# Kernel tuning notes

Measured on AMD Instinct MI355X. Metric: run time of the kernel, lower is better.

## Reference

```python
import jax, jax.numpy as jnp
import numpy as np

D_MODEL, N_LEVELS, N_HEADS, N_POINTS = 256, 4, 8, 4
SHAPES = [(100, 100), (50, 50), (25, 25), (13, 13)]  # (H, W) per level


def setup_inputs() -> dict:
    key = jax.random.key(0)
    ks = jax.random.split(key, 8)
    N = 2
    C = D_MODEL
    Len_in = sum(h * w for h, w in SHAPES)
    Lq = Len_in  # encoder self-attention
    query = jax.random.normal(ks[0], (N, Lq, C), jnp.float32)
    reference_points = jax.random.uniform(ks[1], (N, Lq, N_LEVELS, 2), dtype=jnp.float32)
    input_flatten = jax.random.normal(ks[2], (N, Len_in, C), jnp.float32)
    input_spatial_shapes = np.array(SHAPES, dtype=np.int64)
    areas = input_spatial_shapes[:, 0] * input_spatial_shapes[:, 1]
    input_level_start_index = np.concatenate([[0], np.cumsum(areas)[:-1]]).astype(np.int64)
    s = 1.0 / np.sqrt(C)
    Wv = jax.random.uniform(ks[3], (C, C), jnp.float32, -s, s)
    bv = jnp.zeros((C,), jnp.float32)
    # sampling_offsets: small random weight + the module's grid bias init
    Woff = jax.random.normal(ks[4], (N_HEADS * N_LEVELS * N_POINTS * 2, C), jnp.float32) * 0.01
    thetas = jnp.arange(N_HEADS, dtype=jnp.float32) * (2.0 * np.pi / N_HEADS)
    grid = jnp.stack([jnp.cos(thetas), jnp.sin(thetas)], -1)  # (M,2)
    grid = grid / jnp.max(jnp.abs(grid), axis=-1, keepdims=True)
    grid = jnp.tile(grid[:, None, None, :], (1, N_LEVELS, N_POINTS, 1))
    grid = grid * (jnp.arange(N_POINTS, dtype=jnp.float32) + 1.0)[None, None, :, None]
    boff = grid.reshape(-1)
    Wa = jax.random.normal(ks[5], (N_HEADS * N_LEVELS * N_POINTS, C), jnp.float32) * 0.02
    ba = jnp.zeros((N_HEADS * N_LEVELS * N_POINTS,), jnp.float32)
    Wo = jax.random.uniform(ks[6], (C, C), jnp.float32, -s, s)
    bo = jnp.zeros((C,), jnp.float32)
    return {
        'query': query, 'reference_points': reference_points, 'input_flatten': input_flatten,
        'input_spatial_shapes': input_spatial_shapes, 'input_level_start_index': input_level_start_index,
        'Wv': Wv, 'bv': bv, 'Woff': Woff, 'boff': boff, 'Wa': Wa, 'ba': ba, 'Wo': Wo, 'bo': bo,
    }


def _msda_forward(query, reference_points, input_flatten, shapes, starts,
                  Wv, bv, Woff, boff, Wa, ba, Wo, bo):
    N, Lq, C = query.shape
    M, L, P = N_HEADS, N_LEVELS, N_POINTS
    D = C // M
    value = (input_flatten @ Wv.T + bv).reshape(N, -1, M, D)  # (N, Len_in, M, D)
    off = (query @ Woff.T + boff).reshape(N, Lq, M, L, P, 2)
    attn = jax.nn.softmax((query @ Wa.T + ba).reshape(N, Lq, M, L * P), axis=-1)
    attn = attn.reshape(N, Lq, M, L, P)
    # offset_normalizer = (W_l, H_l)
    norm = jnp.asarray(shapes[:, ::-1].copy(), jnp.float32)  # (L, 2)
    loc = reference_points[:, :, None, :, None, :] + off / norm[None, None, None, :, None, :]
    grids = 2.0 * loc - 1.0  # (N, Lq, M, L, P, 2), grid_sample convention
    out = jnp.zeros((N, Lq, M, D), query.dtype)
    for l in range(L):
        H, W = int(shapes[l, 0]), int(shapes[l, 1])
        s0 = int(starts[l])
        v = value[:, s0:s0 + H * W]  # (N, H*W, M, D)
        # align_corners=False unnormalization
        gx = ((grids[:, :, :, l, :, 0] + 1.0) * W - 1.0) / 2.0  # (N, Lq, M, P)
        gy = ((grids[:, :, :, l, :, 1] + 1.0) * H - 1.0) / 2.0
        x0 = jnp.floor(gx); y0 = jnp.floor(gy)
        fx = gx - x0;       fy = gy - y0
        x0i = x0.astype(jnp.int32); y0i = y0.astype(jnp.int32)

        def gather(iy, ix):
            valid = (iy >= 0) & (iy < H) & (ix >= 0) & (ix < W)
            lin = jnp.clip(iy, 0, H - 1) * W + jnp.clip(ix, 0, W - 1)  # (N, Lq, M, P)
            lin2 = lin.transpose(0, 1, 3, 2).reshape(N, Lq * P, M)
            g = jnp.take_along_axis(v, lin2[..., None], axis=1)  # (N, Lq*P, M, D)
            g = g.reshape(N, Lq, P, M, D).transpose(0, 1, 3, 2, 4)  # (N, Lq, M, P, D)
            return g * valid[..., None]  # zero padding outside

        s00 = gather(y0i, x0i)
        s01 = gather(y0i, x0i + 1)
        s10 = gather(y0i + 1, x0i)
        s11 = gather(y0i + 1, x0i + 1)
        sampled = (s00 * ((1 - fy) * (1 - fx))[..., None] + s01 * ((1 - fy) * fx)[..., None]
                   + s10 * (fy * (1 - fx))[..., None] + s11 * (fy * fx)[..., None])
        out = out + jnp.einsum('nqmp,nqmpd->nqmd', attn[:, :, :, l], sampled)
    out = out.reshape(N, Lq, C)
    return out @ Wo.T + bo


def reference(query, reference_points, input_flatten, input_spatial_shapes, input_level_start_index,
              Wv, bv, Woff, boff, Wa, ba, Wo, bo):
    shapes = np.asarray(input_spatial_shapes)
    starts = np.asarray(input_level_start_index)
    return _msda_forward(query, reference_points, input_flatten, shapes, starts,
                         Wv, bv, Woff, boff, Wa, ba, Wo, bo)
```

## Files before the change

kernel.cpp:

```cpp
#include <hip/hip_runtime.h>
#include <math.h>

#define NB   2
#define LQ   13294
#define NROWS (NB*LQ)
#define CDIM 256

typedef unsigned short u16;
typedef unsigned int   u32;
typedef short bf16x8 __attribute__((ext_vector_type(8)));
typedef float f32x4  __attribute__((ext_vector_type(4)));

struct alignas(8) U16x4 { u16 x, y, z, w; };

__device__ __forceinline__ u16 f2bf(float f) {
    u32 u = __builtin_bit_cast(u32, f);
    u += 0x7FFFu + ((u >> 16) & 1u);
    return (u16)(u >> 16);
}
__device__ __forceinline__ float bf2f(u16 h) {
    u32 u = ((u32)h) << 16;
    return __builtin_bit_cast(float, u);
}

__global__ __launch_bounds__(256)
void prep_all(const float4* __restrict__ query, const float4* __restrict__ inflat,
              const float* __restrict__ Wv, const float* __restrict__ Woff,
              const float* __restrict__ Wa, const float* __restrict__ Wo,
              const float* __restrict__ boff, const float* __restrict__ ba,
              u16* __restrict__ qb, u16* __restrict__ ib,
              u16* __restrict__ wb, float* __restrict__ biascat) {
    const int b = blockIdx.x;
    const int t = threadIdx.x;
    if (b < 6647) {
        int i = b * 256 + t;
        float4 v = query[i];
        U16x4 o{f2bf(v.x), f2bf(v.y), f2bf(v.z), f2bf(v.w)};
        *(U16x4*)&qb[(size_t)i * 4] = o;
    } else if (b < 13294) {
        int i = (b - 6647) * 256 + t;
        float4 v = inflat[i];
        U16x4 o{f2bf(v.x), f2bf(v.y), f2bf(v.z), f2bf(v.w)};
        *(U16x4*)&ib[(size_t)i * 4] = o;
    } else {
        int i = (b - 13294) * 256 + t;
        float v;
        if      (i <  65536) v = Wv[i];
        else if (i < 131072) v = Woff[i - 65536];
        else if (i < 163840) v = Wa[i - 131072];
        else                 v = Wo[i - 163840];
        wb[i] = f2bf(v);
        if (b == 13294) {
            biascat[t] = boff[t];
            if (t < 128) biascat[256 + t] = ba[t];
        }
    }
}

#define GEMM_CORE(A_, B_)                                                     \
    __shared__ u16 Bs[128 * 256];                                             \
    const int tid  = threadIdx.x;                                             \
    const int wave = tid >> 6;                                                \
    const int lane = tid & 63;                                                \
    const int ln16 = lane & 15;                                               \
    const int kq   = lane >> 4;                                               \
    const int row0 = blockIdx.y * 128;                                        \
    const int wr   = (wave >> 1) * 64;                                        \
    const int wc   = (wave & 1) * 64;                                         \
    _Pragma("unroll")                                                         \
    for (int it = 0; it < 16; ++it) {                                         \
        int g  = it * 256 + tid;                                              \
        int c  = g >> 5;                                                      \
        int ch = g & 31;                                                      \
        float4 v = *(const float4*)((B_) + (size_t)c * 256 + ch * 8);         \
        *(float4*)&Bs[c * 256 + (ch ^ (c & 7)) * 8] = v;                      \
    }                                                                         \
    bf16x8 a[4][8];                                                           \
    _Pragma("unroll")                                                         \
    for (int i = 0; i < 4; ++i) {                                             \
        int gr = min(row0 + wr + i * 16 + ln16, M - 1);                       \
        const u16* Ap = (A_) + (size_t)gr * 256 + kq * 8;                     \
        _Pragma("unroll")                                                     \
        for (int kt = 0; kt < 8; ++kt)                                        \
            a[i][kt] = *(const bf16x8*)(Ap + kt * 32);                        \
    }                                                                         \
    __syncthreads();                                                          \
    f32x4 acc[4][4] = {};                                                     \
    _Pragma("unroll")                                                         \
    for (int kt = 0; kt < 8; ++kt) {                                          \
        bf16x8 bfr[4];                                                        \
        _Pragma("unroll")                                                     \
        for (int j = 0; j < 4; ++j) {                                         \
            int c2 = wc + j * 16 + ln16;                                      \
            bfr[j] = *(const bf16x8*)&Bs[c2 * 256 + ((kt * 4 + kq) ^ (c2 & 7)) * 8]; \
        }                                                                     \
        _Pragma("unroll")                                                     \
        for (int i = 0; i < 4; ++i)                                           \
            _Pragma("unroll")                                                 \
            for (int j = 0; j < 4; ++j)                                       \
                acc[i][j] = __builtin_amdgcn_mfma_f32_16x16x32_bf16(          \
                    a[i][kt], bfr[j], acc[i][j], 0, 0, 0);                    \
    }

__global__ __launch_bounds__(256, 2)
void gemm_front(const u16* __restrict__ qb, const u16* __restrict__ ib,
                const u16* __restrict__ wb, const float* __restrict__ bv,
                const float* __restrict__ bcat, u16* __restrict__ value,
                float* __restrict__ offb, float* __restrict__ logit, int M) {
    const int bx = blockIdx.x;
    const u16* Aptr = (bx < 2) ? ib : qb;
    const u16* Bptr = (bx < 2) ? (wb + (size_t)bx * 128 * 256)
                               : (wb + 65536 + (size_t)(bx - 2) * 128 * 256);
    const float* bias = (bx < 2) ? (bv + bx * 128) : (bcat + (bx - 2) * 128);

    GEMM_CORE(Aptr, Bptr)

    #pragma unroll
    for (int j = 0; j < 4; ++j) {
        int lc = wc + j * 16 + ln16;
        float bj = bias[lc];
        #pragma unroll
        for (int i = 0; i < 4; ++i) {
            int gr0 = row0 + wr + i * 16 + kq * 4;
            #pragma unroll
            for (int r = 0; r < 4; ++r) {
                int gr = gr0 + r;
                if (gr < M) {
                    float o = acc[i][j][r] + bj;
                    if (bx < 2)
                        value[(size_t)gr * 256 + bx * 128 + lc] = f2bf(o);
                    else if (bx < 4)
                        offb[(size_t)gr * 256 + (bx - 2) * 128 + lc] = o;
                    else
                        logit[(size_t)gr * 128 + lc] = o;
                }
            }
        }
    }
}

__global__ __launch_bounds__(256, 2)
void gemm_out(const u16* __restrict__ A, const u16* __restrict__ Bw,
              const float* __restrict__ bias, float* __restrict__ C, int M) {
    const u16* Bptr = Bw + (size_t)blockIdx.x * 128 * 256;
    GEMM_CORE(A, Bptr)
    #pragma unroll
    for (int j = 0; j < 4; ++j) {
        int gc = blockIdx.x * 128 + wc + j * 16 + ln16;
        float bj = bias[gc];
        #pragma unroll
        for (int i = 0; i < 4; ++i) {
            int gr0 = row0 + wr + i * 16 + kq * 4;
            #pragma unroll
            for (int r = 0; r < 4; ++r) {
                int gr = gr0 + r;
                if (gr < M) C[(size_t)gr * 256 + gc] = acc[i][j][r] + bj;
            }
        }
    }
}

__global__ __launch_bounds__(256)
void msda_sample(const u16* __restrict__ value,
                 const float* __restrict__ refpts,
                 const float* __restrict__ off,
                 const float* __restrict__ logits,
                 u16* __restrict__ tmp) {
    __shared__ float sAw[4][8][16];
    __shared__ int   sLin[4][8][17][4];
    __shared__ float sW[4][8][17][4];

    const int t  = threadIdx.x;
    const int qb = blockIdx.x * 4;

    if (t < 32) {
        const int qi = t >> 3, m = t & 7;
        const float* lg = logits + (size_t)(qb + qi) * 128 + m * 16;
        float e[16];
        float mx = -1e30f;
        #pragma unroll
        for (int i = 0; i < 16; ++i) { e[i] = lg[i]; mx = fmaxf(mx, e[i]); }
        float s = 0.f;
        #pragma unroll
        for (int i = 0; i < 16; ++i) { e[i] = __expf(e[i] - mx); s += e[i]; }
        const float inv = 1.f / s;
        #pragma unroll
        for (int i = 0; i < 16; ++i) sAw[qi][m][i] = e[i] * inv;
    }
    __syncthreads();

    #pragma unroll
    for (int j2 = 0; j2 < 2; ++j2) {
        const int job = t + j2 * 256;
        const int qi = job >> 7;
        const int m  = (job >> 4) & 7;
        const int p  = job & 15;
        const int l  = p >> 2, pp = p & 3;
        const int q  = qb + qi;
        const int n  = (q >= LQ) ? 1 : 0;

        const int W = (l == 0) ? 100 : (l == 1) ? 50 : (l == 2) ? 25 : 13;
        const int H = W;
        const int st = (l == 0) ? 0 : (l == 1) ? 10000 : (l == 2) ? 12500 : 13125;

        const float rx = refpts[(size_t)q * 8 + l * 2 + 0];
        const float ry = refpts[(size_t)q * 8 + l * 2 + 1];
        const float ox = off[(size_t)q * 256 + m * 32 + (l * 4 + pp) * 2 + 0];
        const float oy = off[(size_t)q * 256 + m * 32 + (l * 4 + pp) * 2 + 1];

        const float locx = rx + ox / (float)W;
        const float locy = ry + oy / (float)H;
        const float grx = 2.f * locx - 1.f;
        const float gry = 2.f * locy - 1.f;
        const float gx = ((grx + 1.f) * (float)W - 1.f) * 0.5f;
        const float gy = ((gry + 1.f) * (float)H - 1.f) * 0.5f;
        const float x0f = floorf(gx), y0f = floorf(gy);
        const float fx = gx - x0f, fy = gy - y0f;
        const int x0 = (int)x0f, y0 = (int)y0f;
        const int x1 = x0 + 1, y1 = y0 + 1;

        const int cx0 = min(max(x0, 0), W - 1);
        const int cx1 = min(max(x1, 0), W - 1);
        const int cy0 = min(max(y0, 0), H - 1);
        const int cy1 = min(max(y1, 0), H - 1);
        const bool vx0 = (x0 >= 0) & (x0 < W);
        const bool vx1 = (x1 >= 0) & (x1 < W);
        const bool vy0 = (y0 >= 0) & (y0 < H);
        const bool vy1 = (y1 >= 0) & (y1 < H);

        const float aw = sAw[qi][m][p];
        const int base = n * LQ + st;
        sLin[qi][m][p][0] = base + cy0 * W + cx0;
        sLin[qi][m][p][1] = base + cy0 * W + cx1;
        sLin[qi][m][p][2] = base + cy1 * W + cx0;
        sLin[qi][m][p][3] = base + cy1 * W + cx1;
        sW[qi][m][p][0] = (vy0 & vx0) ? aw * (1.f - fy) * (1.f - fx) : 0.f;
        sW[qi][m][p][1] = (vy0 & vx1) ? aw * (1.f - fy) * fx         : 0.f;
        sW[qi][m][p][2] = (vy1 & vx0) ? aw * fy * (1.f - fx)         : 0.f;
        sW[qi][m][p][3] = (vy1 & vx1) ? aw * fy * fx                 : 0.f;
    }
    __syncthreads();

    const int qi = t >> 6;
    const int m  = (t >> 3) & 7;
    const int e  = t & 7;
    const int q  = qb + qi;
    const u16* vch = value + m * 32 + e * 4;

    float ax = 0.f, ay = 0.f, az = 0.f, aw_ = 0.f;
    #pragma unroll
    for (int g = 0; g < 4; ++g) {
        U16x4 raw[16];
        float4 Wt4[4];
        #pragma unroll
        for (int pp = 0; pp < 4; ++pp) {
            int p = g * 4 + pp;
            int4 L = *(const int4*)&sLin[qi][m][p][0];
            Wt4[pp] = *(const float4*)&sW[qi][m][p][0];
            raw[pp * 4 + 0] = *(const U16x4*)(vch + (size_t)L.x * 256);
            raw[pp * 4 + 1] = *(const U16x4*)(vch + (size_t)L.y * 256);
            raw[pp * 4 + 2] = *(const U16x4*)(vch + (size_t)L.z * 256);
            raw[pp * 4 + 3] = *(const U16x4*)(vch + (size_t)L.w * 256);
        }
        #pragma unroll
        for (int pp = 0; pp < 4; ++pp) {
            const float* wp = (const float*)&Wt4[pp];
            #pragma unroll
            for (int c = 0; c < 4; ++c) {
                U16x4 r = raw[pp * 4 + c];
                float wgt = wp[c];
                ax  += wgt * bf2f(r.x);
                ay  += wgt * bf2f(r.y);
                az  += wgt * bf2f(r.z);
                aw_ += wgt * bf2f(r.w);
            }
        }
    }
    U16x4 o{f2bf(ax), f2bf(ay), f2bf(az), f2bf(aw_)};
    *(U16x4*)&tmp[(size_t)q * 256 + m * 32 + e * 4] = o;
}

extern "C" void kernel_launch(void* const* d_in, const int* in_sizes, int n_in,
                              void* d_out, int out_size, void* d_ws, size_t ws_size,
                              hipStream_t stream) {
    const float* query  = (const float*)d_in[0];
    const float* refpts = (const float*)d_in[1];
    const float* inflat = (const float*)d_in[2];
    const float* Wv   = (const float*)d_in[5];
    const float* bv   = (const float*)d_in[6];
    const float* Woff = (const float*)d_in[7];
    const float* boff = (const float*)d_in[8];
    const float* Wa   = (const float*)d_in[9];
    const float* ba   = (const float*)d_in[10];
    const float* Wo   = (const float*)d_in[11];
    const float* bo   = (const float*)d_in[12];
    float* out = (float*)d_out;

    char* ws = (char*)d_ws;
    constexpr size_t SZ16 = (size_t)NROWS * 256 * 2;
    constexpr size_t SZ32 = (size_t)NROWS * 256 * 4;
    constexpr size_t SZL  = (size_t)NROWS * 128 * 4;
    u16*   qb    = (u16*)(ws);
    u16*   ib    = (u16*)(ws + SZ16);
    u16*   value = (u16*)(ws + 2 * SZ16);
    float* offb  = (float*)(ws + 3 * SZ16);
    float* logit = (float*)(ws + 3 * SZ16 + SZ32);
    u16*   wb    = (u16*)(ws + 3 * SZ16 + SZ32 + SZL);
    float* bcat  = (float*)(ws + 3 * SZ16 + SZ32 + SZL + 229376 * 2);
    u16*   tmp   = qb;

    dim3 blk(256);
    hipLaunchKernelGGL(prep_all, dim3(14190), blk, 0, stream,
                       (const float4*)query, (const float4*)inflat,
                       Wv, Woff, Wa, Wo, boff, ba, qb, ib, wb, bcat);

    gemm_front<<<dim3(5, 208), blk, 0, stream>>>(
        qb, ib, wb, bv, bcat, value, offb, logit, NROWS);

    hipLaunchKernelGGL(msda_sample, dim3(NROWS / 4), blk, 0, stream,
                       value, refpts, offb, logit, tmp);

    gemm_out<<<dim3(2, 208), blk, 0, stream>>>(
        tmp, wb + 163840, bo, out, NROWS);
}
```

Baseline: 249.1 us.

## Replace LDS-tiled GEMMs with single-wave register-resident B GEMM kernels

Replaces the 256-thread LDS-staged GEMM (128x128 tiles) with a 64-thread single-wave kernel. Each wave holds a 64-column slice of the weight matrix in registers and streams four 16-row A tiles, prefetching the next tile into a double buffer. The fused front GEMM is split into two launches, one for value and one for offsets plus logits, and the output GEMM uses the same kernel. This removes LDS traffic and block-level syncs, at the cost of many more tiny blocks, no sharing of A loads across column blocks, and one extra kernel launch.

```diff
diff --git a/kernel.cpp b/kernel.cpp
--- a/kernel.cpp
+++ b/kernel.cpp
@@ -57,104 +57,70 @@
     }
 }
 
-#define GEMM_CORE(A_, B_)                                                     \
-    __shared__ u16 Bs[128 * 256];                                             \
-    const int tid  = threadIdx.x;                                             \
-    const int wave = tid >> 6;                                                \
-    const int lane = tid & 63;                                                \
-    const int ln16 = lane & 15;                                               \
-    const int kq   = lane >> 4;                                               \
-    const int row0 = blockIdx.y * 128;                                        \
-    const int wr   = (wave >> 1) * 64;                                        \
-    const int wc   = (wave & 1) * 64;                                         \
-    _Pragma("unroll")                                                         \
-    for (int it = 0; it < 16; ++it) {                                         \
-        int g  = it * 256 + tid;                                              \
-        int c  = g >> 5;                                                      \
-        int ch = g & 31;                                                      \
-        float4 v = *(const float4*)((B_) + (size_t)c * 256 + ch * 8);         \
-        *(float4*)&Bs[c * 256 + (ch ^ (c & 7)) * 8] = v;                      \
-    }                                                                         \
-    bf16x8 a[4][8];                                                           \
-    _Pragma("unroll")                                                         \
-    for (int i = 0; i < 4; ++i) {                                             \
-        int gr = min(row0 + wr + i * 16 + ln16, M - 1);                       \
-        const u16* Ap = (A_) + (size_t)gr * 256 + kq * 8;                     \
-        _Pragma("unroll")                                                     \
-        for (int kt = 0; kt < 8; ++kt)                                        \
-            a[i][kt] = *(const bf16x8*)(Ap + kt * 32);                        \
-    }                                                                         \
-    __syncthreads();                                                          \
-    f32x4 acc[4][4] = {};                                                     \
-    _Pragma("unroll")                                                         \
-    for (int kt = 0; kt < 8; ++kt) {                                          \
-        bf16x8 bfr[4];                                                        \
-        _Pragma("unroll")                                                     \
-        for (int j = 0; j < 4; ++j) {                                         \
-            int c2 = wc + j * 16 + ln16;                                      \
-            bfr[j] = *(const bf16x8*)&Bs[c2 * 256 + ((kt * 4 + kq) ^ (c2 & 7)) * 8]; \
-        }                                                                     \
-        _Pragma("unroll")                                                     \
-        for (int i = 0; i < 4; ++i)                                           \
-            _Pragma("unroll")                                                 \
-            for (int j = 0; j < 4; ++j)                                       \
-                acc[i][j] = __builtin_amdgcn_mfma_f32_16x16x32_bf16(          \
-                    a[i][kt], bfr[j], acc[i][j], 0, 0, 0);                    \
-    }
-
-__global__ __launch_bounds__(256, 2)
-void gemm_front(const u16* __restrict__ qb, const u16* __restrict__ ib,
-                const u16* __restrict__ wb, const float* __restrict__ bv,
-                const float* __restrict__ bcat, u16* __restrict__ value,
-                float* __restrict__ offb, float* __restrict__ logit, int M) {
-    const int bx = blockIdx.x;
-    const u16* Aptr = (bx < 2) ? ib : qb;
-    const u16* Bptr = (bx < 2) ? (wb + (size_t)bx * 128 * 256)
-                               : (wb + 65536 + (size_t)(bx - 2) * 128 * 256);
-    const float* bias = (bx < 2) ? (bv + bx * 128) : (bcat + (bx - 2) * 128);
-
-    GEMM_CORE(Aptr, Bptr)
-
+template<int MODE>
+__global__ __launch_bounds__(64, 2)
+void gemm_breg(const u16* __restrict__ A, const u16* __restrict__ Bw,
+               const float* __restrict__ bias, void* __restrict__ C0,
+               float* __restrict__ C1, int M) {
+    const int lane = threadIdx.x;
+    const int ln16 = lane & 15;
+    const int kq   = lane >> 4;
+    const int col0 = blockIdx.x * 64;
+    const int rt0  = blockIdx.y * 64;
+
+    bf16x8 b[4][8];
     #pragma unroll
     for (int j = 0; j < 4; ++j) {
-        int lc = wc + j * 16 + ln16;
-        float bj = bias[lc];
-        #pragma unroll
-        for (int i = 0; i < 4; ++i) {
-            int gr0 = row0 + wr + i * 16 + kq * 4;
+        const u16* Bp = Bw + (size_t)(col0 + j * 16 + ln16) * 256 + kq * 8;
+        #pragma unroll
+        for (int kt = 0; kt < 8; ++kt)
+            b[j][kt] = *(const bf16x8*)(Bp + kt * 32);
+    }
+    float bs[4];
+    #pragma unroll
+    for (int j = 0; j < 4; ++j) bs[j] = bias[col0 + j * 16 + ln16];
+
+    bf16x8 a[2][8];
+    {
+        int gr = min(rt0 + ln16, M - 1);
+        const u16* Ap = A + (size_t)gr * 256 + kq * 8;
+        #pragma unroll
+        for (int kt = 0; kt < 8; ++kt) a[0][kt] = *(const bf16x8*)(Ap + kt * 32);
+    }
+    #pragma unroll
+    for (int rt = 0; rt < 4; ++rt) {
+        if (rt < 3) {
+            int gr = min(rt0 + (rt + 1) * 16 + ln16, M - 1);
+            const u16* Ap = A + (size_t)gr * 256 + kq * 8;
+            #pragma unroll
+            for (int kt = 0; kt < 8; ++kt)
+                a[(rt + 1) & 1][kt] = *(const bf16x8*)(Ap + kt * 32);
+        }
+        f32x4 acc[4] = {};
+        #pragma unroll
+        for (int kt = 0; kt < 8; ++kt)
+            #pragma unroll
+            for (int j = 0; j < 4; ++j)
+                acc[j] = __builtin_amdgcn_mfma_f32_16x16x32_bf16(
+                    a[rt & 1][kt], b[j][kt], acc[j], 0, 0, 0);
+
+        #pragma unroll
+        for (int j = 0; j < 4; ++j) {
+            int gc = col0 + j * 16 + ln16;
             #pragma unroll
             for (int r = 0; r < 4; ++r) {
-                int gr = gr0 + r;
+                int gr = rt0 + rt * 16 + kq * 4 + r;
                 if (gr < M) {
-                    float o = acc[i][j][r] + bj;
-                    if (bx < 2)
-                        value[(size_t)gr * 256 + bx * 128 + lc] = f2bf(o);
-                    else if (bx < 4)
-                        offb[(size_t)gr * 256 + (bx - 2) * 128 + lc] = o;
-                    else
-                        logit[(size_t)gr * 128 + lc] = o;
+                    float o = acc[j][r] + bs[j];
+                    if (MODE == 0)
+                        ((u16*)C0)[(size_t)gr * 256 + gc] = f2bf(o);
+                    else if (MODE == 2)
+                        ((float*)C0)[(size_t)gr * 256 + gc] = o;
+                    else {
+                        if (gc < 256) ((float*)C0)[(size_t)gr * 256 + gc] = o;
+                        else          C1[(size_t)gr * 128 + (gc - 256)] = o;
+                    }
                 }
-            }
-        }
-    }
-}
-
-__global__ __launch_bounds__(256, 2)
-void gemm_out(const u16* __restrict__ A, const u16* __restrict__ Bw,
-              const float* __restrict__ bias, float* __restrict__ C, int M) {
-    const u16* Bptr = Bw + (size_t)blockIdx.x * 128 * 256;
-    GEMM_CORE(A, Bptr)
-    #pragma unroll
-    for (int j = 0; j < 4; ++j) {
-        int gc = blockIdx.x * 128 + wc + j * 16 + ln16;
-        float bj = bias[gc];
-        #pragma unroll
-        for (int i = 0; i < 4; ++i) {
-            int gr0 = row0 + wr + i * 16 + kq * 4;
-            #pragma unroll
-            for (int r = 0; r < 4; ++r) {
-                int gr = gr0 + r;
-                if (gr < M) C[(size_t)gr * 256 + gc] = acc[i][j][r] + bj;
             }
         }
     }
@@ -309,17 +275,20 @@
     float* bcat  = (float*)(ws + 3 * SZ16 + SZ32 + SZL + 229376 * 2);
     u16*   tmp   = qb;
 
-    dim3 blk(256);
-    hipLaunchKernelGGL(prep_all, dim3(14190), blk, 0, stream,
+    const int RG = (NROWS + 63) / 64;
+
+    hipLaunchKernelGGL(prep_all, dim3(14190), dim3(256), 0, stream,
                        (const float4*)query, (const float4*)inflat,
                        Wv, Woff, Wa, Wo, boff, ba, qb, ib, wb, bcat);
 
-    gemm_front<<<dim3(5, 208), blk, 0, stream>>>(
-        qb, ib, wb, bv, bcat, value, offb, logit, NROWS);
-
-    hipLaunchKernelGGL(msda_sample, dim3(NROWS / 4), blk, 0, stream,
+    gemm_breg<0><<<dim3(4, RG), dim3(64), 0, stream>>>(
+        ib, wb, bv, (void*)value, nullptr, NROWS);
+    gemm_breg<1><<<dim3(6, RG), dim3(64), 0, stream>>>(
+        qb, wb + 65536, bcat, (void*)offb, logit, NROWS);
+
+    hipLaunchKernelGGL(msda_sample, dim3(NROWS / 4), dim3(256), 0, stream,
                        value, refpts, offb, logit, tmp);
 
-    gemm_out<<<dim3(2, 208), blk, 0, stream>>>(
-        tmp, wb + 163840, bo, out, NROWS);
-}
+    gemm_breg<2><<<dim3(4, RG), dim3(64), 0, stream>>>(
+        tmp, wb + 163840, bo, (void*)out, nullptr, NROWS);
+}
```

Measured after the change: 245.8 us. Within noise of the previous version (-1.3%).
